# Performance work log

Hardware: AMD Instinct MI355X
Metric: run time of the kernel (lower is better)

Reference implementation:

```python
import jax, jax.numpy as jnp
import numpy as np
import math

B, N, D = 4, 4096, 256


def setup_inputs() -> dict:
    key = jax.random.key(0)
    k0, k1, k2, k3 = jax.random.split(key, 4)
    # kaiming-uniform-like init for the square weight matrices
    bound = math.sqrt(6.0 / D)
    return {
        "x": jax.random.normal(k0, (B, N, D), dtype=jnp.float32),
        "Wq": jax.random.uniform(k1, (D, D), dtype=jnp.float32, minval=-bound, maxval=bound),
        "Wk": jax.random.uniform(k2, (D, D), dtype=jnp.float32, minval=-bound, maxval=bound),
        "Wv": jax.random.uniform(k3, (D, D), dtype=jnp.float32, minval=-bound, maxval=bound),
    }


def reference(x, Wq, Wk, Wv):
    # x: [B, N, D]; W*: [D, D]
    q = x @ Wq.T
    k = x @ Wk.T
    v = x @ Wv.T
    n = x.shape[1]
    d_k = x.shape[2]
    # mask = triu(ones, diagonal=1): 1 strictly above the diagonal.
    # (1 - mask) is 1 on and below the diagonal, so those positions get -1e10
    # (faithful to the original: it masks the diagonal and past, keeps future).
    mask = jnp.triu(jnp.ones((n, n), dtype=x.dtype), k=1)
    scale = jnp.asarray(1.0 / math.sqrt(d_k), dtype=x.dtype)
    s = (jnp.einsum('bnd,bmd->bnm', q, k) - (1.0 - mask) * 1e10) * scale
    # Faithful quirk: softmax over dim=1 (the query/row axis), not the last axis.
    s = jax.nn.softmax(s, axis=1)
    return jnp.einsum('bnm,bmd->bnd', s, v)
```

## Files before the change

kernel.cpp:

```cpp
#include <hip/hip_runtime.h>
#include <hip/hip_bf16.h>


typedef float f32x4 __attribute__((ext_vector_type(4)));
typedef __bf16 bf16x8 __attribute__((ext_vector_type(8)));
typedef __bf16 bf16x4 __attribute__((ext_vector_type(4)));

#define MFMA16(a, b, c) __builtin_amdgcn_mfma_f32_16x16x32_bf16((a), (b), (c), 0, 0, 0)

constexpr int SEQ = 4096;
constexpr int DIM = 256;

__device__ __forceinline__ void gl16(const __bf16* g, __bf16* l) {
  __builtin_amdgcn_global_load_lds((const __attribute__((address_space(1))) void*)g,
                                   (__attribute__((address_space(3))) void*)l, 16, 0, 0);
}

__global__ void k_prep(const float* __restrict__ Wq, const float* __restrict__ Wk,
                       const float* __restrict__ Wv, __bf16* __restrict__ Wb,
                       float* __restrict__ colsum) {
  int i = blockIdx.x * 256 + threadIdx.x;
  if (i < 3 * 65536) {
    const float* src = (i < 65536) ? Wq : (i < 131072 ? Wk : Wv);
    Wb[i] = (__bf16)src[i & 65535];
  }
  if (i < 4 * SEQ) colsum[i] = 0.f;
}

__global__ __launch_bounds__(256, 2) void k_qkv(const float* __restrict__ x,
                                                const __bf16* __restrict__ Wb,
                                                __bf16* __restrict__ Qb,
                                                __bf16* __restrict__ Kb,
                                                __bf16* __restrict__ Vb) {
  __shared__ __bf16 wsh[64][264];
  const int t = threadIdx.x, lane = t & 63, w = t >> 6;
  const int ln = lane & 15, quad = lane >> 4, q8 = quad * 8;
  const int i0 = blockIdx.x * 64;
  bf16x8 xa[8];
#pragma unroll
  for (int kf = 0; kf < 8; ++kf) {
    const float* src = &x[(size_t)(i0 + w * 16 + ln) * DIM + kf * 32 + q8];
    float4 v0 = *(const float4*)&src[0];
    float4 v1 = *(const float4*)&src[4];
    xa[kf] = bf16x8{(__bf16)v0.x, (__bf16)v0.y, (__bf16)v0.z, (__bf16)v0.w,
                    (__bf16)v1.x, (__bf16)v1.y, (__bf16)v1.z, (__bf16)v1.w};
  }
  for (int zj = 0; zj < 12; ++zj) {
    const int z = zj >> 2, j0 = (zj & 3) * 64;
    const __bf16* W = Wb + z * 65536 + j0 * 256;
    bf16x8 stg[8];
#pragma unroll
    for (int i = 0; i < 8; ++i) stg[i] = *(const bf16x8*)&W[(t + i * 256) * 8];
    __syncthreads();
#pragma unroll
    for (int i = 0; i < 8; ++i)
      *(bf16x8*)&wsh[(t >> 5) + i * 8][(t & 31) * 8] = stg[i];
    __syncthreads();
    f32x4 acc[4] = {};
#pragma unroll
    for (int kf = 0; kf < 8; ++kf) {
      bf16x8 bb[4];
#pragma unroll
      for (int tj = 0; tj < 4; ++tj)
        bb[tj] = *(bf16x8*)&wsh[tj * 16 + ln][kf * 32 + q8];
#pragma unroll
      for (int tj = 0; tj < 4; ++tj) acc[tj] = MFMA16(xa[kf], bb[tj], acc[tj]);
    }
    __bf16* Out = (z == 0) ? Qb : (z == 1 ? Kb : Vb);
#pragma unroll
    for (int tj = 0; tj < 4; ++tj)
#pragma unroll
      for (int r = 0; r < 4; ++r) {
        int row = i0 + w * 16 + quad * 4 + r;
        int col = j0 + tj * 16 + ln;
        Out[(size_t)row * DIM + col] = (__bf16)acc[tj][r];
      }
  }
}

__global__ __launch_bounds__(256, 2) void k_colsum(const __bf16* __restrict__ Qb,
                                                   const __bf16* __restrict__ Kb,
                                                   float* __restrict__ colsum) {
  __shared__ __bf16 qs[64][264];
  const int t = threadIdx.x, lane = t & 63, w = t >> 6;
  const int ln = lane & 15, quad = lane >> 4, q8 = quad * 8;
  const int bid = blockIdx.x;
  const int b = (bid & 7) >> 1;
  const int i = ((bid >> 3) << 1) | (bid & 1);
  const int round = i >> 6, k = i & 63;
  const int mt = round ? 31 - (k & 31) : (k & 31);
  const int s = (k >> 5) | (round << 1);
  const int m0 = mt * 128;
  const __bf16* Qp = Qb + (size_t)b * SEQ * DIM;
  const __bf16* Kp = Kb + (size_t)b * SEQ * DIM;
  bf16x8 kb[2][8];
#pragma unroll
  for (int tm = 0; tm < 2; ++tm)
#pragma unroll
    for (int kf = 0; kf < 8; ++kf)
      kb[tm][kf] = *(const bf16x8*)&Kp[(size_t)(m0 + w * 32 + tm * 16 + ln) * DIM + kf * 32 + q8];
  float csum[2] = {0.f, 0.f};
  for (int nc = s; nc < 2 * mt + 2; nc += 4) {
    bf16x8 stg[8];
    const __bf16* src = Qp + (size_t)nc * 64 * DIM;
#pragma unroll
    for (int i2 = 0; i2 < 8; ++i2) stg[i2] = *(const bf16x8*)&src[(t + i2 * 256) * 8];
    __syncthreads();
#pragma unroll
    for (int i2 = 0; i2 < 8; ++i2)
      *(bf16x8*)&qs[(t >> 5) + i2 * 8][(t & 31) * 8] = stg[i2];
    __syncthreads();
    f32x4 acc[4][2] = {};
#pragma unroll
    for (int kf = 0; kf < 8; ++kf) {
      bf16x8 aa[4];
#pragma unroll
      for (int tn = 0; tn < 4; ++tn) aa[tn] = *(bf16x8*)&qs[tn * 16 + ln][kf * 32 + q8];
#pragma unroll
      for (int tn = 0; tn < 4; ++tn)
#pragma unroll
        for (int tm = 0; tm < 2; ++tm)
          acc[tn][tm] = MFMA16(aa[tn], kb[tm][kf], acc[tn][tm]);
    }
#pragma unroll
    for (int tn = 0; tn < 4; ++tn)
#pragma unroll
      for (int tm = 0; tm < 2; ++tm)
#pragma unroll
        for (int r = 0; r < 4; ++r) {
          int n_g = nc * 64 + tn * 16 + quad * 4 + r;
          int m_g = m0 + w * 32 + tm * 16 + ln;
          if (n_g < m_g) csum[tm] += __expf(acc[tn][tm][r] * 0.0625f);
        }
  }
#pragma unroll
  for (int tm = 0; tm < 2; ++tm) {
    float v = csum[tm];
    v += __shfl_xor(v, 16);
    v += __shfl_xor(v, 32);
    if (quad == 0)
      atomicAdd(&colsum[b * SEQ + m0 + w * 32 + tm * 16 + ln], v);
  }
}

__global__ void k_vpt(const __bf16* __restrict__ Vb, const float* __restrict__ colsum,
                      __bf16* __restrict__ VpT) {
  __shared__ __bf16 tile[64][72];
  const int t = threadIdx.x;
  const int b = blockIdx.z;
  const int m0 = blockIdx.x * 64, d0 = blockIdx.y * 64;
  {
    int row = t >> 2, part = t & 3;
    float cs = colsum[b * SEQ + m0 + row];
    float inv = (m0 + row == 0) ? (1.0f / 4096.0f) : (1.0f / cs);
#pragma unroll
    for (int i = 0; i < 2; ++i) {
      int c = part * 2 + i;
      bf16x8 v = *(const bf16x8*)&Vb[(size_t)(b * SEQ + m0 + row) * DIM + d0 + c * 8];
      bf16x8 o;
#pragma unroll
      for (int j = 0; j < 8; ++j) o[j] = (__bf16)((float)v[j] * inv);
      *(bf16x8*)&tile[row][c * 8] = o;
    }
  }
  __syncthreads();
  {
    int row = t >> 2, part = t & 3;
#pragma unroll
    for (int i = 0; i < 2; ++i) {
      int c = part * 2 + i;
      bf16x8 o;
#pragma unroll
      for (int j = 0; j < 8; ++j) o[j] = tile[c * 8 + j][row];
      *(bf16x8*)&VpT[(size_t)((b * 64 + blockIdx.x) * 256 + d0 + row) * 64 + c * 8] = o;
    }
  }
}

__global__ __launch_bounds__(256, 2) void k_attn(const __bf16* __restrict__ Qb,
                                                 const __bf16* __restrict__ Kb,
                                                 const __bf16* __restrict__ Vt_blk,
                                                 const __bf16* __restrict__ Vb,
                                                 __bf16* __restrict__ opart,
                                                 float* __restrict__ out_f32,
                                                 int nsplit, int fuse) {
  __shared__ __bf16 ksh[64 * 256];
  __shared__ __bf16 vsm[256 * 64];
  __shared__ __bf16 ps[64 * 72];
  const int t = threadIdx.x, lane = t & 63, w = t >> 6;
  const int ln = lane & 15, quad = lane >> 4, q8 = quad * 8;
  const int wn = w & 1;
  const int wm = w >> 1;
  const int bid = blockIdx.x;
  const int b = (bid & 7) >> 1;
  const int i = ((bid >> 3) << 1) | (bid & 1);
  int nt, s;
  if (nsplit == 1) {
    nt = i & 63; s = 0;
  } else {
    int round = i >> 6, k = i & 63;
    nt = (round & 1) ? 63 - k : k;
    s = round;
  }
  const int n0 = nt * 64;
  const __bf16* Qp = Qb + (size_t)b * SEQ * DIM;
  const __bf16* Kp = Kb + (size_t)b * SEQ * DIM;
  const __bf16* Vt = Vt_blk + (size_t)b * SEQ * DIM;
  bf16x8 qf[2][8];
#pragma unroll
  for (int tn = 0; tn < 2; ++tn)
#pragma unroll
    for (int kf = 0; kf < 8; ++kf)
      qf[tn][kf] = *(const bf16x8*)&Qp[(size_t)(n0 + wn * 32 + tn * 16 + ln) * DIM + kf * 32 + q8];
  auto stageK = [&](int msv) {
    const __bf16* kp = Kp + (size_t)msv * 16384;
#pragma unroll
    for (int i2 = 0; i2 < 8; ++i2) {
      int sl = t + i2 * 256;
      int row = sl >> 5, g = sl & 31;
      gl16(&kp[row * 256 + ((g ^ (row & 15)) << 3)], &ksh[sl * 8]);
    }
  };
  auto stageV = [&](int msv) {
    const __bf16* vp = Vt + (size_t)msv * 16384;
#pragma unroll
    for (int i2 = 0; i2 < 8; ++i2) {
      int sl = t + i2 * 256;
      int d = sl >> 3, g = sl & 7;
      gl16(&vp[d * 64 + ((g ^ (d & 7)) << 3)], &vsm[sl * 8]);
    }
  };
  f32x4 accO[2][8] = {};
  const int msEnd = nt;
  int ms = 63 - s;
  if (ms >= msEnd) { stageK(ms); stageV(ms); }
  __syncthreads();
  for (; ms >= msEnd; ms -= nsplit) {
    const int msn = ms - nsplit;
    f32x4 accS[2][2] = {};
#pragma unroll
    for (int kf = 0; kf < 8; ++kf) {
      bf16x8 bb[2];
#pragma unroll
      for (int tm = 0; tm < 2; ++tm) {
        int row = wm * 32 + tm * 16 + ln;
        bb[tm] = *(const bf16x8*)&ksh[row * 256 + (((kf * 4 + quad) ^ ln) << 3)];
      }
#pragma unroll
      for (int tn = 0; tn < 2; ++tn)
#pragma unroll
        for (int tm = 0; tm < 2; ++tm)
          accS[tn][tm] = MFMA16(qf[tn][kf], bb[tm], accS[tn][tm]);
    }
    __syncthreads();
    if (msn >= msEnd) stageK(msn);
#pragma unroll
    for (int tn = 0; tn < 2; ++tn)
#pragma unroll
      for (int tm = 0; tm < 2; ++tm) {
        int ml = wm * 32 + tm * 16 + ln;
        int m_g = ms * 64 + ml;
#pragma unroll
        for (int r = 0; r < 4; ++r) {
          int nl = wn * 32 + tn * 16 + quad * 4 + r;
          float e = (n0 + nl >= m_g) ? 0.f : __expf(accS[tn][tm][r] * 0.0625f);
          ps[nl * 72 + ml] = (__bf16)e;
        }
      }
    __syncthreads();
#pragma unroll
    for (int kf = 0; kf < 2; ++kf) {
      bf16x8 aa[2];
#pragma unroll
      for (int tn = 0; tn < 2; ++tn)
        aa[tn] = *(const bf16x8*)&ps[(wn * 32 + tn * 16 + ln) * 72 + kf * 32 + q8];
#pragma unroll
      for (int td = 0; td < 8; ++td) {
        int d = wm * 128 + td * 16 + ln;
        bf16x8 bb = *(const bf16x8*)&vsm[d * 64 + (((kf * 4 + quad) ^ (ln & 7)) << 3)];
#pragma unroll
        for (int tn = 0; tn < 2; ++tn) accO[tn][td] = MFMA16(aa[tn], bb, accO[tn][td]);
      }
    }
    __syncthreads();
    if (msn >= msEnd) stageV(msn);
    __syncthreads();
  }
  if (fuse) {
    const __bf16* V0 = Vb + (size_t)b * SEQ * DIM;
    float* Op = out_f32 + (size_t)b * SEQ * DIM;
#pragma unroll
    for (int tn = 0; tn < 2; ++tn)
#pragma unroll
      for (int td = 0; td < 8; ++td) {
        int col = wm * 128 + td * 16 + ln;
        float c0 = (float)V0[col] * (1.0f / 4096.0f);
#pragma unroll
        for (int r = 0; r < 4; ++r) {
          int row = n0 + wn * 32 + tn * 16 + quad * 4 + r;
          Op[(size_t)row * DIM + col] = accO[tn][td][r] + c0;
        }
      }
  } else {
    __bf16* P = opart + (size_t)s * (4u << 20) + ((size_t)b << 20);
#pragma unroll
    for (int tn = 0; tn < 2; ++tn)
#pragma unroll
      for (int td = 0; td < 8; ++td) {
        int col = wm * 128 + td * 16 + ln;
#pragma unroll
        for (int r = 0; r < 4; ++r) {
          int row = n0 + wn * 32 + tn * 16 + quad * 4 + r;
          P[(size_t)row * DIM + col] = (__bf16)accO[tn][td][r];
        }
      }
  }
}

__global__ void k_final(const __bf16* __restrict__ opart, const __bf16* __restrict__ Vb,
                        float* __restrict__ out, int nsplit) {
  const size_t base = ((size_t)blockIdx.x * 256 + threadIdx.x) * 8;
  const int b = (int)(base >> 20);
  const int d0 = (int)(base & 255);
  float sum[8] = {};
  for (int s = 0; s < nsplit; ++s) {
    bf16x8 v = *(const bf16x8*)&opart[(size_t)s * (4u << 20) + base];
#pragma unroll
    for (int j = 0; j < 8; ++j) sum[j] += (float)v[j];
  }
  bf16x8 v0 = *(const bf16x8*)&Vb[((size_t)b << 20) + d0];
  float4 o0, o1;
  o0.x = sum[0] + (float)v0[0] * (1.0f / 4096.0f);
  o0.y = sum[1] + (float)v0[1] * (1.0f / 4096.0f);
  o0.z = sum[2] + (float)v0[2] * (1.0f / 4096.0f);
  o0.w = sum[3] + (float)v0[3] * (1.0f / 4096.0f);
  o1.x = sum[4] + (float)v0[4] * (1.0f / 4096.0f);
  o1.y = sum[5] + (float)v0[5] * (1.0f / 4096.0f);
  o1.z = sum[6] + (float)v0[6] * (1.0f / 4096.0f);
  o1.w = sum[7] + (float)v0[7] * (1.0f / 4096.0f);
  *(float4*)&out[base] = o0;
  *(float4*)&out[base + 4] = o1;
}

extern "C" void kernel_launch(void* const* d_in, const int* in_sizes, int n_in,
                              void* d_out, int out_size, void* d_ws, size_t ws_size,
                              hipStream_t stream) {
  const float* x = (const float*)d_in[0];
  const float* Wq = (const float*)d_in[1];
  const float* Wk = (const float*)d_in[2];
  const float* Wv = (const float*)d_in[3];
  float* out = (float*)d_out;
  char* ws = (char*)d_ws;
  __bf16* Qb = (__bf16*)(ws);
  __bf16* Kb = (__bf16*)(ws + (8u << 20));
  __bf16* Vb = (__bf16*)(ws + (16u << 20));
  __bf16* VpT = (__bf16*)(ws + (24u << 20));
  float* colsum = (float*)(ws + (32u << 20));
  __bf16* Wb = (__bf16*)(ws + (32u << 20) + (1u << 16));
  const size_t base = (32u << 20) + (1u << 16) + (384u << 10);
  __bf16* opart = (__bf16*)(ws + base);
  int nsplit = 1;
  if (ws_size >= base + 4u * (8u << 20)) nsplit = 4;
  else if (ws_size >= base + 2u * (8u << 20)) nsplit = 2;
  const int fuse = (nsplit == 1);

  k_prep<<<dim3(768), dim3(256), 0, stream>>>(Wq, Wk, Wv, Wb, colsum);
  k_qkv<<<dim3(256), dim3(256), 0, stream>>>(x, Wb, Qb, Kb, Vb);
  k_colsum<<<dim3(512), dim3(256), 0, stream>>>(Qb, Kb, colsum);
  k_vpt<<<dim3(64, 4, 4), dim3(256), 0, stream>>>(Vb, colsum, VpT);
  k_attn<<<dim3(256 * nsplit), dim3(256), 0, stream>>>(Qb, Kb, VpT, Vb, opart, out,
                                                       nsplit, fuse);
  if (!fuse)
    k_final<<<dim3(2048), dim3(256), 0, stream>>>(opart, Vb, out, nsplit);
}
```

Baseline: 208.6 us.

## Double-buffer Q tiles via direct global-to-LDS loads with swizzle in colsum

Restructures the column-sum kernel to work on 64-key tiles instead of 128, doubling the grid. Q chunks are now staged with direct global-to-LDS loads into two buffers, with an XOR swizzle to avoid bank conflicts, so the next chunk loads while the current one computes. The goal is to overlap memory traffic with MFMA work and to balance load across the triangular work. In exchange, LDS use doubles (64KB) and each block keeps fewer K registers.

```diff
diff --git a/kernel.cpp b/kernel.cpp
--- a/kernel.cpp
+++ b/kernel.cpp
@@ -81,66 +81,60 @@
 __global__ __launch_bounds__(256, 2) void k_colsum(const __bf16* __restrict__ Qb,
                                                    const __bf16* __restrict__ Kb,
                                                    float* __restrict__ colsum) {
-  __shared__ __bf16 qs[64][264];
+  __shared__ __bf16 qsh[2 * 64 * 256];
   const int t = threadIdx.x, lane = t & 63, w = t >> 6;
   const int ln = lane & 15, quad = lane >> 4, q8 = quad * 8;
   const int bid = blockIdx.x;
   const int b = (bid & 7) >> 1;
   const int i = ((bid >> 3) << 1) | (bid & 1);
   const int round = i >> 6, k = i & 63;
-  const int mt = round ? 31 - (k & 31) : (k & 31);
-  const int s = (k >> 5) | (round << 1);
-  const int m0 = mt * 128;
+  const int mt = (round & 1) ? 63 - k : k;
+  const int s = round;
+  const int m0 = mt * 64;
   const __bf16* Qp = Qb + (size_t)b * SEQ * DIM;
   const __bf16* Kp = Kb + (size_t)b * SEQ * DIM;
-  bf16x8 kb[2][8];
-#pragma unroll
-  for (int tm = 0; tm < 2; ++tm)
-#pragma unroll
-    for (int kf = 0; kf < 8; ++kf)
-      kb[tm][kf] = *(const bf16x8*)&Kp[(size_t)(m0 + w * 32 + tm * 16 + ln) * DIM + kf * 32 + q8];
-  float csum[2] = {0.f, 0.f};
-  for (int nc = s; nc < 2 * mt + 2; nc += 4) {
-    bf16x8 stg[8];
-    const __bf16* src = Qp + (size_t)nc * 64 * DIM;
-#pragma unroll
-    for (int i2 = 0; i2 < 8; ++i2) stg[i2] = *(const bf16x8*)&src[(t + i2 * 256) * 8];
-    __syncthreads();
-#pragma unroll
-    for (int i2 = 0; i2 < 8; ++i2)
-      *(bf16x8*)&qs[(t >> 5) + i2 * 8][(t & 31) * 8] = stg[i2];
-    __syncthreads();
-    f32x4 acc[4][2] = {};
+  bf16x8 kb[8];
+#pragma unroll
+  for (int kf = 0; kf < 8; ++kf)
+    kb[kf] = *(const bf16x8*)&Kp[(size_t)(m0 + w * 16 + ln) * DIM + kf * 32 + q8];
+  auto stageq = [&](int ncv, int buf) {
+    const __bf16* src = Qp + (size_t)ncv * 16384;
+#pragma unroll
+    for (int i2 = 0; i2 < 8; ++i2) {
+      int sl = t + i2 * 256;
+      int row = sl >> 5, g = sl & 31;
+      gl16(&src[row * 256 + ((g ^ (row & 15)) << 3)], &qsh[buf * 16384 + sl * 8]);
+    }
+  };
+  float csum = 0.f;
+  int nc = s, cur = 0;
+  if (nc <= mt) stageq(nc, 0);
+  for (; nc <= mt; nc += 4, cur ^= 1) {
+    __syncthreads();
+    if (nc + 4 <= mt) stageq(nc + 4, cur ^ 1);
+    f32x4 acc[4] = {};
 #pragma unroll
     for (int kf = 0; kf < 8; ++kf) {
-      bf16x8 aa[4];
-#pragma unroll
-      for (int tn = 0; tn < 4; ++tn) aa[tn] = *(bf16x8*)&qs[tn * 16 + ln][kf * 32 + q8];
-#pragma unroll
-      for (int tn = 0; tn < 4; ++tn)
-#pragma unroll
-        for (int tm = 0; tm < 2; ++tm)
-          acc[tn][tm] = MFMA16(aa[tn], kb[tm][kf], acc[tn][tm]);
-    }
+#pragma unroll
+      for (int tn = 0; tn < 4; ++tn) {
+        int row = tn * 16 + ln;
+        bf16x8 af = *(const bf16x8*)&qsh[cur * 16384 + row * 256 +
+                                         (((kf * 4 + quad) ^ ln) << 3)];
+        acc[tn] = MFMA16(af, kb[kf], acc[tn]);
+      }
+    }
+    const int m_g = m0 + w * 16 + ln;
 #pragma unroll
     for (int tn = 0; tn < 4; ++tn)
 #pragma unroll
-      for (int tm = 0; tm < 2; ++tm)
-#pragma unroll
-        for (int r = 0; r < 4; ++r) {
-          int n_g = nc * 64 + tn * 16 + quad * 4 + r;
-          int m_g = m0 + w * 32 + tm * 16 + ln;
-          if (n_g < m_g) csum[tm] += __expf(acc[tn][tm][r] * 0.0625f);
-        }
-  }
-#pragma unroll
-  for (int tm = 0; tm < 2; ++tm) {
-    float v = csum[tm];
-    v += __shfl_xor(v, 16);
-    v += __shfl_xor(v, 32);
-    if (quad == 0)
-      atomicAdd(&colsum[b * SEQ + m0 + w * 32 + tm * 16 + ln], v);
-  }
+      for (int r = 0; r < 4; ++r) {
+        int n_g = nc * 64 + tn * 16 + quad * 4 + r;
+        if (n_g < m_g) csum += __expf(acc[tn][r] * 0.0625f);
+      }
+  }
+  csum += __shfl_xor(csum, 16);
+  csum += __shfl_xor(csum, 32);
+  if (quad == 0) atomicAdd(&colsum[b * SEQ + m0 + w * 16 + ln], csum);
 }
 
 __global__ void k_vpt(const __bf16* __restrict__ Vb, const float* __restrict__ colsum,
@@ -366,7 +360,7 @@
 
   k_prep<<<dim3(768), dim3(256), 0, stream>>>(Wq, Wk, Wv, Wb, colsum);
   k_qkv<<<dim3(256), dim3(256), 0, stream>>>(x, Wb, Qb, Kb, Vb);
-  k_colsum<<<dim3(512), dim3(256), 0, stream>>>(Qb, Kb, colsum);
+  k_colsum<<<dim3(1024), dim3(256), 0, stream>>>(Qb, Kb, colsum);
   k_vpt<<<dim3(64, 4, 4), dim3(256), 0, stream>>>(Vb, colsum, VpT);
   k_attn<<<dim3(256 * nsplit), dim3(256), 0, stream>>>(Qb, Kb, VpT, Vb, opart, out,
                                                        nsplit, fuse);
```

Result: no change. 204.9 us (-1.8%).
